# Optimization experiments

Measured on AMD Instinct MI355X. Metric: run time of the kernel, lower is better.

## Reference

```python
import jax, jax.numpy as jnp
import numpy as np

BN_EPS = 1e-5
# regular 3x3 kernel grid offsets: row0 = dy, row1 = dx, kernel positions in row-major order
REG = jnp.array([[-1, -1, -1, 0, 0, 0, 1, 1, 1],
                 [-1,  0,  1, -1, 0, 1, -1, 0, 1]], dtype=jnp.float32)


def conv3x3(x, w, b):
    y = jax.lax.conv_general_dilated(x, w, window_strides=(1, 1),
                                     padding=((1, 1), (1, 1)),
                                     dimension_numbers=('NCHW', 'OIHW', 'NCHW'))
    return y + b[None, :, None, None]


def deform_conv3x3(x, dy, dx, w):
    # x: [N,C,H,W]; dy,dx: [N,9,H,W] per-kernel-tap offsets; w: [O,C,3,3]
    N, C, H, W = x.shape
    K = 9
    ky = jnp.repeat(jnp.arange(3), 3)   # [0,0,0,1,1,1,2,2,2]
    kx = jnp.tile(jnp.arange(3), 3)     # [0,1,2,0,1,2,0,1,2]
    # sampling positions: p = p_out - pad + k*dilation + offset (stride=1, pad=dil=1)
    py = dy + (jnp.arange(H) - 1)[None, None, :, None] + ky[None, :, None, None].astype(x.dtype)
    px = dx + (jnp.arange(W) - 1)[None, None, None, :] + kx[None, :, None, None].astype(x.dtype)
    y0 = jnp.floor(py)
    x0 = jnp.floor(px)
    wy = py - y0  # bilinear weights
    wx = px - x0
    y0i = y0.astype(jnp.int32)
    x0i = x0.astype(jnp.int32)
    nidx = jnp.arange(N)[:, None, None, None]

    def gather(yi, xi):
        valid = ((yi >= 0) & (yi < H) & (xi >= 0) & (xi < W)).astype(x.dtype)
        v = x[nidx, :, jnp.clip(yi, 0, H - 1), jnp.clip(xi, 0, W - 1)]  # [N,K,H,W,C]
        return v * valid[..., None]

    sampled = (gather(y0i,     x0i)     * ((1 - wy) * (1 - wx))[..., None]
             + gather(y0i,     x0i + 1) * ((1 - wy) * wx)[..., None]
             + gather(y0i + 1, x0i)     * (wy * (1 - wx))[..., None]
             + gather(y0i + 1, x0i + 1) * (wy * wx)[..., None])  # [N,K,H,W,C]
    O = w.shape[0]
    return jnp.einsum('nkhwc,ock->nohw', sampled, w.reshape(O, C, K))


def setup_inputs() -> dict:
    key = jax.random.key(0)
    ks = jax.random.split(key, 12)
    N, C, H, W = 2, 256, 96, 96
    O = 256
    sc = 1.0 / np.sqrt(C * 9)
    return {
        'x': jax.random.normal(ks[0], (N, C, H, W), jnp.float32),
        'mask_attention': jax.random.normal(ks[1], (N, C, H, W), jnp.float32),
        'w_tm': jax.random.normal(ks[2], (4, C, 3, 3), jnp.float32) * sc,
        'b_tm': jax.random.normal(ks[3], (4,), jnp.float32) * 0.01,
        'w_tr': jax.random.normal(ks[4], (2, C, 3, 3), jnp.float32) * sc,
        'b_tr': jax.random.normal(ks[5], (2,), jnp.float32) * 0.01,
        'w_deform': jax.random.normal(ks[6], (O, C, 3, 3), jnp.float32) * sc,
        'bn_gamma': jnp.ones((O,), jnp.float32),
        'bn_beta': jnp.zeros((O,), jnp.float32),
        'bn_mean': jax.random.normal(ks[7], (O,), jnp.float32) * 0.01,
        'bn_var': jax.random.uniform(ks[8], (O,), jnp.float32, 0.5, 1.5),
    }


def reference(x, mask_attention, w_tm, b_tm, w_tr, b_tr, w_deform,
              bn_gamma, bn_beta, bn_mean, bn_var):
    # mask_attention is overwritten by x in the original forward; ignored.
    N, C, H, W = x.shape
    tm = conv3x3(x, w_tm, b_tm)                       # [N,4,H,W]
    T = tm.transpose(0, 2, 3, 1).reshape(N, H, W, 2, 2)
    off = jnp.einsum('nhwij,jk->nhwik', T, REG) - REG  # [N,H,W,2,9], (T-I)@REG
    tr = conv3x3(x, w_tr, b_tr)                        # [N,2,H,W]
    off = off + tr.transpose(0, 2, 3, 1)[..., None]    # broadcast translation to all 9 taps
    dy = off[..., 0, :].transpose(0, 3, 1, 2)          # [N,9,H,W]
    dx = off[..., 1, :].transpose(0, 3, 1, 2)
    out = deform_conv3x3(x, dy, dx, w_deform)          # [N,O,H,W]
    inv = jax.lax.rsqrt(bn_var + BN_EPS)
    out = (out - bn_mean[None, :, None, None]) * (inv * bn_gamma)[None, :, None, None] \
          + bn_beta[None, :, None, None]
    return jax.nn.relu(out + x)
```

## Files before the change

kernel.cpp:

```cpp
#include <hip/hip_runtime.h>
#include <stdint.h>

#define H_ 96
#define W_ 96
#define C_ 256
#define O_ 256
#define N_ 2
#define HW_ (H_*W_)
#define M_ (N_*HW_)
#define GK 2304

typedef _Float16 f16x8 __attribute__((ext_vector_type(8)));
typedef _Float16 f16x2 __attribute__((ext_vector_type(2)));
typedef float f32x4 __attribute__((ext_vector_type(4)));
typedef unsigned short us4 __attribute__((ext_vector_type(4)));
typedef unsigned short us8 __attribute__((ext_vector_type(8)));

__device__ __forceinline__ unsigned short f2h(float f) {
  union { _Float16 h; unsigned short u; } v;
  v.h = (_Float16)f;
  return v.u;
}
__device__ __forceinline__ f16x2 hpair(float f) {
  const _Float16 h = (_Float16)f;
  return (f16x2){h, h};
}

__global__ __launch_bounds__(256) void k_pre(const float* __restrict__ x,
                                             const float* __restrict__ w_df,
                                             const float* __restrict__ w_tm,
                                             const float* __restrict__ w_tr,
                                             unsigned short* __restrict__ xt,
                                             unsigned short* __restrict__ wfrag,
                                             unsigned short* __restrict__ w6p) {
  const int b = blockIdx.x;
  const int tid = threadIdx.x;
  if (b < 576) {
    __shared__ unsigned short tile[64][130];
    const int pt = b % 144;
    const int ch = (b / 144) & 1;
    const int n  = b / 288;
    const int p0 = pt * 64, c0 = ch * 128;
    const float* xp = x + (size_t)n * C_ * HW_;
    unsigned short* xtp = xt + (size_t)n * C_ * HW_;
    const int tx = tid & 15, ty = tid >> 4;
#pragma unroll
    for (int pass = 0; pass < 8; pass++) {
      const int c = pass * 16 + ty;
      const f32x4 v = *(const f32x4*)(xp + (size_t)(c0 + c) * HW_ + p0 + tx * 4);
#pragma unroll
      for (int i = 0; i < 4; i++) tile[tx * 4 + i][c] = f2h(v[i]);
    }
    __syncthreads();
    const int l32 = tid & 31, pr = tid >> 5;
#pragma unroll
    for (int pass = 0; pass < 8; pass++) {
      const int p = pass * 8 + pr;
      us4 v;
#pragma unroll
      for (int i = 0; i < 4; i++) v[i] = tile[p][l32 * 4 + i];
      *(us4*)(xtp + (size_t)(p0 + p) * C_ + c0 + l32 * 4) = v;
    }
  } else if (b < 864) {
    const int base = (b - 576) * 2048 + tid * 8;
    const int l  = (base >> 3) & 63;
    const int g  = (base >> 9) & 15;
    const int ks = (base >> 13) & 7;
    const int t  = base >> 16;
    const int o  = g * 16 + (l & 15);
    const int c  = ks * 32 + (l >> 4) * 8;
    us8 res;
#pragma unroll
    for (int j = 0; j < 8; j++) res[j] = f2h(w_df[(size_t)(o * 256 + c + j) * 9 + t]);
    *(us8*)(wfrag + base) = res;
  } else {
    int idx = (b - 864) * 256 + tid;
    int t = idx >> 12;
    int r = idx & 4095;
    int j = r >> 8;
    int c = r & 255;
    float v = 0.f;
    if (j < 4) v = w_tm[(size_t)(j * C_ + c) * 9 + t];
    else if (j < 6) v = w_tr[(size_t)((j - 4) * C_ + c) * 9 + t];
    w6p[idx] = f2h(v);
  }
}

__global__ __launch_bounds__(512, 2) void k_fused(const unsigned short* __restrict__ xt,
                                                  const unsigned short* __restrict__ Wfrag,
                                                  const unsigned short* __restrict__ w6p,
                                                  const float* __restrict__ b_tm,
                                                  const float* __restrict__ b_tr,
                                                  const float* __restrict__ xres,
                                                  const float* __restrict__ gamma,
                                                  const float* __restrict__ beta,
                                                  const float* __restrict__ mean,
                                                  const float* __restrict__ var,
                                                  float* __restrict__ out) {
  __shared__ unsigned short As[2][80 * 256] __attribute__((aligned(16)));
  __shared__ float sred5[5][8][16][8];
  __shared__ float coords_s[80][9][2];
  __shared__ int   nofs[80];
  const int tid = threadIdx.x;
  const int wave = tid >> 6, lane = tid & 63;
  const int row = lane & 15, quad = lane >> 4;
  const int pb = (blockIdx.x & 7) * 32 + (blockIdx.x >> 3);
  const bool fat = pb < 128;
  const int nt = fat ? 5 : 4;
  const int m0 = fat ? pb * 80 : 10240 + (pb - 128) * 64;
  const int sr = tid >> 4;
  const int cg = tid & 15;

#pragma unroll
  for (int t5 = 0; t5 < 5; ++t5) {
    if (t5 < nt) {
      const int ts = m0 + t5 * 16;
      const int nn = ts / HW_;
      const int hw = ts - nn * HW_;
      const int h = hw / W_, w0 = hw - h * W_;
      const unsigned short* xts = xt + (size_t)nn * C_ * HW_;
      const int cq = wave * 32;
      f32x4 oacc = {0.f, 0.f, 0.f, 0.f};
      const f16x8 zero8 = {};
#pragma unroll
      for (int t = 0; t < 9; t++) {
        const int ty = t / 3, tx = t % 3;
        const int y = h + ty - 1;
        if (y < 0 || y >= H_) continue;
        const int xx = w0 + row + tx - 1;
        const bool valid = (xx >= 0) && (xx < W_);
        const int xc = min(max(xx, 0), W_ - 1);
        f16x8 av = *(const f16x8*)(const void*)(xts + (size_t)(y * W_ + xc) * C_ + cq + quad * 8);
        if (!valid) av = zero8;
        const f16x8 bv = *(const f16x8*)(const void*)(w6p + (size_t)(t * 16 + row) * C_ + cq + quad * 8);
        oacc = __builtin_amdgcn_mfma_f32_16x16x32_f16(av, bv, oacc, 0, 0, 0);
      }
      if (row < 6) {
#pragma unroll
        for (int r = 0; r < 4; r++) sred5[t5][wave][quad * 4 + r][row] = oacc[r];
      }
    }
  }
  __syncthreads();
  if (tid < nt * 16) {
    const int rg = tid;
    const int gm = m0 + rg;
    const int nn = gm / HW_;
    const int hw = gm - nn * HW_;
    const int h = hw / W_, w = hw - h * W_;
    const int tt = rg >> 4, mm = rg & 15;
    float a[6];
#pragma unroll
    for (int j = 0; j < 6; j++) {
      float s = 0.f;
#pragma unroll
      for (int wv = 0; wv < 8; wv++) s += sred5[tt][wv][mm][j];
      a[j] = s;
    }
    const float tm0 = a[0] + b_tm[0];
    const float tm1 = a[1] + b_tm[1];
    const float tm2 = a[2] + b_tm[2];
    const float tm3 = a[3] + b_tm[3];
    const float tr0 = a[4] + b_tr[0];
    const float tr1 = a[5] + b_tr[1];
#pragma unroll
    for (int t = 0; t < 9; t++) {
      const float ry = (float)(t / 3) - 1.f;
      const float rx = (float)(t % 3) - 1.f;
      coords_s[rg][t][0] = (float)h + tr0 + tm0 * ry + tm1 * rx;
      coords_s[rg][t][1] = (float)w + tr1 + tm2 * ry + tm3 * rx;
    }
    nofs[rg] = nn * (C_ * HW_);
  }
  __syncthreads();

  f32x4 acc[5][2] = {};
  float cwA[4], cwB[4];
  us8 uA0[4], uA1[4], uB0[4], uB1[4];

#define ISSUE(S, R, TAP)                                                       \
  {                                                                            \
    const int r_ = (R);                                                        \
    const int nof = nofs[r_];                                                  \
    const float py = coords_s[r_][TAP][0];                                     \
    const float px = coords_s[r_][TAP][1];                                     \
    const float fy = floorf(py), fx = floorf(px);                              \
    const float wy = py - fy, wx = px - fx;                                    \
    const int y0 = (int)fy, x0 = (int)fx;                                      \
    const int y1 = y0 + 1, x1 = x0 + 1;                                        \
    const float vy0 = (y0 >= 0 && y0 < H_) ? 1.f : 0.f;                        \
    const float vy1 = (y1 >= 0 && y1 < H_) ? 1.f : 0.f;                        \
    const float vx0 = (x0 >= 0 && x0 < W_) ? 1.f : 0.f;                        \
    const float vx1 = (x1 >= 0 && x1 < W_) ? 1.f : 0.f;                        \
    cw##S[0] = (1.f - wy) * (1.f - wx) * vy0 * vx0;                            \
    cw##S[1] = (1.f - wy) * wx * vy0 * vx1;                                    \
    cw##S[2] = wy * (1.f - wx) * vy1 * vx0;                                    \
    cw##S[3] = wy * wx * vy1 * vx1;                                            \
    const int cy0 = min(max(y0, 0), H_ - 1), cy1 = min(max(y1, 0), H_ - 1);    \
    const int cx0 = min(max(x0, 0), W_ - 1), cx1 = min(max(x1, 0), W_ - 1);    \
    const int b0 = nof + (cy0 * W_ + cx0) * C_ + cg * 16;                      \
    const int b1 = nof + (cy0 * W_ + cx1) * C_ + cg * 16;                      \
    const int b2 = nof + (cy1 * W_ + cx0) * C_ + cg * 16;                      \
    const int b3 = nof + (cy1 * W_ + cx1) * C_ + cg * 16;                      \
    u##S##0[0] = *(const us8*)(xt + b0); u##S##1[0] = *(const us8*)(xt + b0 + 8); \
    u##S##0[1] = *(const us8*)(xt + b1); u##S##1[1] = *(const us8*)(xt + b1 + 8); \
    u##S##0[2] = *(const us8*)(xt + b2); u##S##1[2] = *(const us8*)(xt + b2 + 8); \
    u##S##0[3] = *(const us8*)(xt + b3); u##S##1[3] = *(const us8*)(xt + b3 + 8); \
  }

#define LERPW(S, R, ASB)                                                       \
  {                                                                            \
    const int r_ = (R);                                                        \
    const f16x2 c0 = hpair(cw##S[0]), c1 = hpair(cw##S[1]);                    \
    const f16x2 c2 = hpair(cw##S[2]), c3 = hpair(cw##S[3]);                    \
    us8 r0v, r1v;                                                              \
    {                                                                          \
      const f16x2* p0 = (const f16x2*)&u##S##0[0];                             \
      const f16x2* p1 = (const f16x2*)&u##S##0[1];                             \
      const f16x2* p2 = (const f16x2*)&u##S##0[2];                             \
      const f16x2* p3 = (const f16x2*)&u##S##0[3];                             \
      f16x2* d = (f16x2*)&r0v;                                                 \
      _Pragma("unroll")                                                        \
      for (int p = 0; p < 4; p++) {                                            \
        f16x2 r = p0[p] * c0; r = p1[p] * c1 + r;                              \
        r = p2[p] * c2 + r;   r = p3[p] * c3 + r;  d[p] = r;                   \
      }                                                                        \
    }                                                                          \
    {                                                                          \
      const f16x2* p0 = (const f16x2*)&u##S##1[0];                             \
      const f16x2* p1 = (const f16x2*)&u##S##1[1];                             \
      const f16x2* p2 = (const f16x2*)&u##S##1[2];                             \
      const f16x2* p3 = (const f16x2*)&u##S##1[3];                             \
      f16x2* d = (f16x2*)&r1v;                                                 \
      _Pragma("unroll")                                                        \
      for (int p = 0; p < 4; p++) {                                            \
        f16x2 r = p0[p] * c0; r = p1[p] * c1 + r;                              \
        r = p2[p] * c2 + r;   r = p3[p] * c3 + r;  d[p] = r;                   \
      }                                                                        \
    }                                                                          \
    const int q0i = cg * 2, q1i = cg * 2 + 1;                                  \
    const int s0 = (q0i & 24) | ((q0i ^ r_) & 7);                              \
    const int s1 = (q1i & 24) | ((q1i ^ r_) & 7);                              \
    *(us8*)(void*)&ASB[r_ * 256 + s0 * 8] = r0v;                               \
    *(us8*)(void*)&ASB[r_ * 256 + s1 * 8] = r1v;                               \
  }

  const bool third = fat && (sr < 16);

  ISSUE(A, sr, 0);
  __builtin_amdgcn_sched_barrier(0);

  for (int tap = 0; tap < 9; tap++) {
    unsigned short* __restrict__ asb = &As[tap & 1][0];

    ISSUE(B, sr + 32, tap);
    const unsigned short* wfTap =
        Wfrag + (size_t)tap * 65536 + wave * 1024 + lane * 8;
    f16x8 bv[2];
#pragma unroll
    for (int ot = 0; ot < 2; ot++) bv[ot] = *(const f16x8*)(const void*)(wfTap + ot * 512);
    __builtin_amdgcn_sched_barrier(0);

    LERPW(A, sr, asb);
    if (third) {
      ISSUE(A, sr + 64, tap);
      __builtin_amdgcn_sched_barrier(0);
    }
    LERPW(B, sr + 32, asb);
    if (third) LERPW(A, sr + 64, asb);

    __syncthreads();

    if (tap < 8) {
      ISSUE(A, sr, tap + 1);
      __builtin_amdgcn_sched_barrier(0);
    }

#pragma unroll
    for (int ks = 0; ks < 8; ks++) {
      const int q = ks * 4 + quad;
      const int slot = (q & 24) | ((q ^ row) & 7);
      f16x8 a0 = *(const f16x8*)(const void*)&asb[(0 * 16 + row) * 256 + slot * 8];
      f16x8 a1 = *(const f16x8*)(const void*)&asb[(1 * 16 + row) * 256 + slot * 8];
      f16x8 a2 = *(const f16x8*)(const void*)&asb[(2 * 16 + row) * 256 + slot * 8];
      f16x8 a3 = *(const f16x8*)(const void*)&asb[(3 * 16 + row) * 256 + slot * 8];
      f16x8 a4;
      if (fat) a4 = *(const f16x8*)(const void*)&asb[(4 * 16 + row) * 256 + slot * 8];
      f16x8 bn[2];
      if (ks < 7) {
        const unsigned short* wfn = wfTap + (size_t)(ks + 1) * 8192;
#pragma unroll
        for (int ot = 0; ot < 2; ot++) bn[ot] = *(const f16x8*)(const void*)(wfn + ot * 512);
      }
#pragma unroll
      for (int ot = 0; ot < 2; ot++) {
        acc[0][ot] = __builtin_amdgcn_mfma_f32_16x16x32_f16(a0, bv[ot], acc[0][ot], 0, 0, 0);
        acc[1][ot] = __builtin_amdgcn_mfma_f32_16x16x32_f16(a1, bv[ot], acc[1][ot], 0, 0, 0);
        acc[2][ot] = __builtin_amdgcn_mfma_f32_16x16x32_f16(a2, bv[ot], acc[2][ot], 0, 0, 0);
        acc[3][ot] = __builtin_amdgcn_mfma_f32_16x16x32_f16(a3, bv[ot], acc[3][ot], 0, 0, 0);
      }
      if (fat) {
#pragma unroll
        for (int ot = 0; ot < 2; ot++)
          acc[4][ot] = __builtin_amdgcn_mfma_f32_16x16x32_f16(a4, bv[ot], acc[4][ot], 0, 0, 0);
      }
      if (ks < 7) {
#pragma unroll
        for (int ot = 0; ot < 2; ot++) bv[ot] = bn[ot];
      }
    }
  }

#pragma unroll
  for (int ot = 0; ot < 2; ot++) {
    const int o = wave * 32 + ot * 16 + row;
    const float sc = rsqrtf(var[o] + 1e-5f) * gamma[o];
    const float bi = beta[o] - mean[o] * sc;
#pragma unroll
    for (int t5 = 0; t5 < 5; t5++) {
      if (t5 < nt) {
        const int ts = m0 + t5 * 16;
        const int nn = ts / HW_;
        const int hw0 = ts - nn * HW_ + quad * 4;
        const size_t ob = (size_t)(nn * O_ + o) * HW_ + hw0;
        const f32x4 rv = *(const f32x4*)(xres + ob);
        f32x4 ov;
#pragma unroll
        for (int r = 0; r < 4; r++) ov[r] = fmaxf(acc[t5][ot][r] * sc + bi + rv[r], 0.f);
        *(f32x4*)(out + ob) = ov;
      }
    }
  }
}

extern "C" void kernel_launch(void* const* d_in, const int* in_sizes, int n_in,
                              void* d_out, int out_size, void* d_ws, size_t ws_size,
                              hipStream_t stream) {
  const float* x     = (const float*)d_in[0];
  const float* w_tm  = (const float*)d_in[2];
  const float* b_tm  = (const float*)d_in[3];
  const float* w_tr  = (const float*)d_in[4];
  const float* b_tr  = (const float*)d_in[5];
  const float* w_df  = (const float*)d_in[6];
  const float* gamma = (const float*)d_in[7];
  const float* beta  = (const float*)d_in[8];
  const float* mean  = (const float*)d_in[9];
  const float* var   = (const float*)d_in[10];
  float* out = (float*)d_out;

  char* ws = (char*)d_ws;
  unsigned short* xt    = (unsigned short*)(ws);
  unsigned short* wfrag = (unsigned short*)(ws + 9437184);
  unsigned short* w6p   = (unsigned short*)(ws + 9437184 + 1179648);

  k_pre<<<1008, 256, 0, stream>>>(x, w_df, w_tm, w_tr, xt, wfrag, w6p);
  k_fused<<<256, 512, 0, stream>>>(xt, wfrag, w6p, b_tm, b_tr, x,
                                   gamma, beta, mean, var, out);
}
```

Baseline: 165.7 us.

## Double block to 1024 threads splitting M tiles across two wave halves

Launches the fused kernel with 1024 threads per block, giving 16 waves. Each half of the waves owns a subset of the 16-row M tiles (3+2 or 2+2) while keeping the same 8-way output-channel split. The bilinear gather and LDS staging are now spread over twice as many threads, so each thread fills one row (plus a third for fat blocks) instead of two or three, and per-thread accumulator and register state shrinks. The B-fragment prefetch becomes a two-deep ping-pong. The trade-off is that each weight fragment is now loaded twice per block, once per half, and the MFMA work per wave shrinks, which may reduce latency hiding per wave.

```diff
diff --git a/kernel.cpp b/kernel.cpp
--- a/kernel.cpp
+++ b/kernel.cpp
@@ -86,40 +86,43 @@
   }
 }
 
-__global__ __launch_bounds__(512, 2) void k_fused(const unsigned short* __restrict__ xt,
-                                                  const unsigned short* __restrict__ Wfrag,
-                                                  const unsigned short* __restrict__ w6p,
-                                                  const float* __restrict__ b_tm,
-                                                  const float* __restrict__ b_tr,
-                                                  const float* __restrict__ xres,
-                                                  const float* __restrict__ gamma,
-                                                  const float* __restrict__ beta,
-                                                  const float* __restrict__ mean,
-                                                  const float* __restrict__ var,
-                                                  float* __restrict__ out) {
+__global__ __launch_bounds__(1024) void k_fused(const unsigned short* __restrict__ xt,
+                                                const unsigned short* __restrict__ Wfrag,
+                                                const unsigned short* __restrict__ w6p,
+                                                const float* __restrict__ b_tm,
+                                                const float* __restrict__ b_tr,
+                                                const float* __restrict__ xres,
+                                                const float* __restrict__ gamma,
+                                                const float* __restrict__ beta,
+                                                const float* __restrict__ mean,
+                                                const float* __restrict__ var,
+                                                float* __restrict__ out) {
   __shared__ unsigned short As[2][80 * 256] __attribute__((aligned(16)));
   __shared__ float sred5[5][8][16][8];
   __shared__ float coords_s[80][9][2];
   __shared__ int   nofs[80];
   const int tid = threadIdx.x;
   const int wave = tid >> 6, lane = tid & 63;
+  const int w7 = wave & 7, half = wave >> 3;
   const int row = lane & 15, quad = lane >> 4;
   const int pb = (blockIdx.x & 7) * 32 + (blockIdx.x >> 3);
   const bool fat = pb < 128;
   const int nt = fat ? 5 : 4;
   const int m0 = fat ? pb * 80 : 10240 + (pb - 128) * 64;
+  const int tb  = half ? (fat ? 3 : 2) : 0;
+  const int ntw = half ? 2 : (fat ? 3 : 2);
   const int sr = tid >> 4;
   const int cg = tid & 15;
 
 #pragma unroll
   for (int t5 = 0; t5 < 5; ++t5) {
-    if (t5 < nt) {
+    if (t5 < nt && (t5 & 1) == half) {
       const int ts = m0 + t5 * 16;
       const int nn = ts / HW_;
       const int hw = ts - nn * HW_;
       const int h = hw / W_, w0 = hw - h * W_;
       const unsigned short* xts = xt + (size_t)nn * C_ * HW_;
-      const int cq = wave * 32;
+      const int cq = w7 * 32;
       f32x4 oacc = {0.f, 0.f, 0.f, 0.f};
       const f16x8 zero8 = {};
 #pragma unroll
@@ -137,7 +140,7 @@
       }
       if (row < 6) {
 #pragma unroll
-        for (int r = 0; r < 4; r++) sred5[t5][wave][quad * 4 + r][row] = oacc[r];
+        for (int r = 0; r < 4; r++) sred5[t5][w7][quad * 4 + r][row] = oacc[r];
       }
     }
   }
@@ -174,11 +177,11 @@
   }
   __syncthreads();
 
-  f32x4 acc[5][2] = {};
-  float cwA[4], cwB[4];
-  us8 uA0[4], uA1[4], uB0[4], uB1[4];
-
-#define ISSUE(S, R, TAP)                                                       \
+  f32x4 acc[3][2] = {};
+  float cwA[4];
+  us8 uA0[4], uA1[4];
+
+#define ISSUE(R, TAP)                                                          \
   {                                                                            \
     const int r_ = (R);                                                        \
     const int nof = nofs[r_];                                                  \
@@ -192,33 +195,33 @@
     const float vy1 = (y1 >= 0 && y1 < H_) ? 1.f : 0.f;                        \
     const float vx0 = (x0 >= 0 && x0 < W_) ? 1.f : 0.f;                        \
     const float vx1 = (x1 >= 0 && x1 < W_) ? 1.f : 0.f;                        \
-    cw##S[0] = (1.f - wy) * (1.f - wx) * vy0 * vx0;                            \
-    cw##S[1] = (1.f - wy) * wx * vy0 * vx1;                                    \
-    cw##S[2] = wy * (1.f - wx) * vy1 * vx0;                                    \
-    cw##S[3] = wy * wx * vy1 * vx1;                                            \
+    cwA[0] = (1.f - wy) * (1.f - wx) * vy0 * vx0;                              \
+    cwA[1] = (1.f - wy) * wx * vy0 * vx1;                                      \
+    cwA[2] = wy * (1.f - wx) * vy1 * vx0;                                      \
+    cwA[3] = wy * wx * vy1 * vx1;                                              \
     const int cy0 = min(max(y0, 0), H_ - 1), cy1 = min(max(y1, 0), H_ - 1);    \
     const int cx0 = min(max(x0, 0), W_ - 1), cx1 = min(max(x1, 0), W_ - 1);    \
     const int b0 = nof + (cy0 * W_ + cx0) * C_ + cg * 16;                      \
     const int b1 = nof + (cy0 * W_ + cx1) * C_ + cg * 16;                      \
     const int b2 = nof + (cy1 * W_ + cx0) * C_ + cg * 16;                      \
     const int b3 = nof + (cy1 * W_ + cx1) * C_ + cg * 16;                      \
-    u##S##0[0] = *(const us8*)(xt + b0); u##S##1[0] = *(const us8*)(xt + b0 + 8); \
-    u##S##0[1] = *(const us8*)(xt + b1); u##S##1[1] = *(const us8*)(xt + b1 + 8); \
-    u##S##0[2] = *(const us8*)(xt + b2); u##S##1[2] = *(const us8*)(xt + b2 + 8); \
-    u##S##0[3] = *(const us8*)(xt + b3); u##S##1[3] = *(const us8*)(xt + b3 + 8); \
-  }
-
-#define LERPW(S, R, ASB)                                                       \
+    uA0[0] = *(const us8*)(xt + b0); uA1[0] = *(const us8*)(xt + b0 + 8);      \
+    uA0[1] = *(const us8*)(xt + b1); uA1[1] = *(const us8*)(xt + b1 + 8);      \
+    uA0[2] = *(const us8*)(xt + b2); uA1[2] = *(const us8*)(xt + b2 + 8);      \
+    uA0[3] = *(const us8*)(xt + b3); uA1[3] = *(const us8*)(xt + b3 + 8);      \
+  }
+
+#define LERPW(R, ASB)                                                          \
   {                                                                            \
     const int r_ = (R);                                                        \
-    const f16x2 c0 = hpair(cw##S[0]), c1 = hpair(cw##S[1]);                    \
-    const f16x2 c2 = hpair(cw##S[2]), c3 = hpair(cw##S[3]);                    \
+    const f16x2 c0 = hpair(cwA[0]), c1 = hpair(cwA[1]);                        \
+    const f16x2 c2 = hpair(cwA[2]), c3 = hpair(cwA[3]);                        \
     us8 r0v, r1v;                                                              \
     {                                                                          \
-      const f16x2* p0 = (const f16x2*)&u##S##0[0];                             \
-      const f16x2* p1 = (const f16x2*)&u##S##0[1];                             \
-      const f16x2* p2 = (const f16x2*)&u##S##0[2];                             \
-      const f16x2* p3 = (const f16x2*)&u##S##0[3];                             \
+      const f16x2* p0 = (const f16x2*)&uA0[0];                                 \
+      const f16x2* p1 = (const f16x2*)&uA0[1];                                 \
+      const f16x2* p2 = (const f16x2*)&uA0[2];                                 \
+      const f16x2* p3 = (const f16x2*)&uA0[3];                                 \
       f16x2* d = (f16x2*)&r0v;                                                 \
       _Pragma("unroll")                                                        \
       for (int p = 0; p < 4; p++) {                                            \
@@ -227,10 +230,10 @@
       }                                                                        \
     }                                                                          \
     {                                                                          \
-      const f16x2* p0 = (const f16x2*)&u##S##1[0];                             \
-      const f16x2* p1 = (const f16x2*)&u##S##1[1];                             \
-      const f16x2* p2 = (const f16x2*)&u##S##1[2];                             \
-      const f16x2* p3 = (const f16x2*)&u##S##1[3];                             \
+      const f16x2* p0 = (const f16x2*)&uA1[0];                                 \
+      const f16x2* p1 = (const f16x2*)&uA1[1];                                 \
+      const f16x2* p2 = (const f16x2*)&uA1[2];                                 \
+      const f16x2* p3 = (const f16x2*)&uA1[3];                                 \
       f16x2* d = (f16x2*)&r1v;                                                 \
       _Pragma("unroll")                                                        \
       for (int p = 0; p < 4; p++) {                                            \
@@ -245,80 +248,80 @@
     *(us8*)(void*)&ASB[r_ * 256 + s1 * 8] = r1v;                               \
   }
 
+#define GS(KS, BX, BY)                                                         \
+  {                                                                            \
+    const int q = (KS) * 4 + quad;                                             \
+    const int slot = (q & 24) | ((q ^ row) & 7);                               \
+    f16x8 a0 = *(const f16x8*)(const void*)&asb[((tb + 0) * 16 + row) * 256 + slot * 8]; \
+    f16x8 a1 = *(const f16x8*)(const void*)&asb[((tb + 1) * 16 + row) * 256 + slot * 8]; \
+    f16x8 a2;                                                                  \
+    if (ntw > 2) a2 = *(const f16x8*)(const void*)&asb[((tb + 2) * 16 + row) * 256 + slot * 8]; \
+    f16x8 nx, ny;                                                              \
+    if ((KS) < 6) {                                                            \
+      const unsigned short* wfn = wfTap + (size_t)((KS) + 2) * 8192;           \
+      nx = *(const f16x8*)(const void*)(wfn);                                  \
+      ny = *(const f16x8*)(const void*)(wfn + 512);                            \
+    }                                                                          \
+    acc[0][0] = __builtin_amdgcn_mfma_f32_16x16x32_f16(a0, BX, acc[0][0], 0, 0, 0); \
+    acc[0][1] = __builtin_amdgcn_mfma_f32_16x16x32_f16(a0, BY, acc[0][1], 0, 0, 0); \
+    acc[1][0] = __builtin_amdgcn_mfma_f32_16x16x32_f16(a1, BX, acc[1][0], 0, 0, 0); \
+    acc[1][1] = __builtin_amdgcn_mfma_f32_16x16x32_f16(a1, BY, acc[1][1], 0, 0, 0); \
+    if (ntw > 2) {                                                             \
+      acc[2][0] = __builtin_amdgcn_mfma_f32_16x16x32_f16(a2, BX, acc[2][0], 0, 0, 0); \
+      acc[2][1] = __builtin_amdgcn_mfma_f32_16x16x32_f16(a2, BY, acc[2][1], 0, 0, 0); \
+    }                                                                          \
+    if ((KS) < 6) { BX = nx; BY = ny; }                                        \
+  }
+
   const bool third = fat && (sr < 16);
 
-  ISSUE(A, sr, 0);
+  ISSUE(sr, 0);
   __builtin_amdgcn_sched_barrier(0);
 
   for (int tap = 0; tap < 9; tap++) {
     unsigned short* __restrict__ asb = &As[tap & 1][0];
-
-    ISSUE(B, sr + 32, tap);
     const unsigned short* wfTap =
-        Wfrag + (size_t)tap * 65536 + wave * 1024 + lane * 8;
-    f16x8 bv[2];
-#pragma unroll
-    for (int ot = 0; ot < 2; ot++) bv[ot] = *(const f16x8*)(const void*)(wfTap + ot * 512);
+        Wfrag + (size_t)tap * 65536 + w7 * 1024 + lane * 8;
+
+    f16x8 B0 = *(const f16x8*)(const void*)(wfTap);
+    f16x8 B1 = *(const f16x8*)(const void*)(wfTap + 512);
+    f16x8 B2 = *(const f16x8*)(const void*)(wfTap + 8192);
+    f16x8 B3 = *(const f16x8*)(const void*)(wfTap + 8704);
     __builtin_amdgcn_sched_barrier(0);
 
-    LERPW(A, sr, asb);
+    LERPW(sr, asb);
     if (third) {
-      ISSUE(A, sr + 64, tap);
+      ISSUE(sr + 64, tap);
       __builtin_amdgcn_sched_barrier(0);
-    }
-    LERPW(B, sr + 32, asb);
-    if (third) LERPW(A, sr + 64, asb);
+      LERPW(sr + 64, asb);
+    }
 
     __syncthreads();
 
     if (tap < 8) {
-      ISSUE(A, sr, tap + 1);
+      ISSUE(sr, tap + 1);
       __builtin_amdgcn_sched_barrier(0);
     }
 
-#pragma unroll
-    for (int ks = 0; ks < 8; ks++) {
-      const int q = ks * 4 + quad;
-      const int slot = (q & 24) | ((q ^ row) & 7);
-      f16x8 a0 = *(const f16x8*)(const void*)&asb[(0 * 16 + row) * 256 + slot * 8];
-      f16x8 a1 = *(const f16x8*)(const void*)&asb[(1 * 16 + row) * 256 + slot * 8];
-      f16x8 a2 = *(const f16x8*)(const void*)&asb[(2 * 16 + row) * 256 + slot * 8];
-      f16x8 a3 = *(const f16x8*)(const void*)&asb[(3 * 16 + row) * 256 + slot * 8];
-      f16x8 a4;
-      if (fat) a4 = *(const f16x8*)(const void*)&asb[(4 * 16 + row) * 256 + slot * 8];
-      f16x8 bn[2];
-      if (ks < 7) {
-        const unsigned short* wfn = wfTap + (size_t)(ks + 1) * 8192;
-#pragma unroll
-        for (int ot = 0; ot < 2; ot++) bn[ot] = *(const f16x8*)(const void*)(wfn + ot * 512);
-      }
-#pragma unroll
-      for (int ot = 0; ot < 2; ot++) {
-        acc[0][ot] = __builtin_amdgcn_mfma_f32_16x16x32_f16(a0, bv[ot], acc[0][ot], 0, 0, 0);
-        acc[1][ot] = __builtin_amdgcn_mfma_f32_16x16x32_f16(a1, bv[ot], acc[1][ot], 0, 0, 0);
-        acc[2][ot] = __builtin_amdgcn_mfma_f32_16x16x32_f16(a2, bv[ot], acc[2][ot], 0, 0, 0);
-        acc[3][ot] = __builtin_amdgcn_mfma_f32_16x16x32_f16(a3, bv[ot], acc[3][ot], 0, 0, 0);
-      }
-      if (fat) {
-#pragma unroll
-        for (int ot = 0; ot < 2; ot++)
-          acc[4][ot] = __builtin_amdgcn_mfma_f32_16x16x32_f16(a4, bv[ot], acc[4][ot], 0, 0, 0);
-      }
-      if (ks < 7) {
-#pragma unroll
-        for (int ot = 0; ot < 2; ot++) bv[ot] = bn[ot];
-      }
-    }
+    GS(0, B0, B1)
+    GS(1, B2, B3)
+    GS(2, B0, B1)
+    GS(3, B2, B3)
+    GS(4, B0, B1)
+    GS(5, B2, B3)
+    GS(6, B0, B1)
+    GS(7, B2, B3)
   }
 
 #pragma unroll
   for (int ot = 0; ot < 2; ot++) {
-    const int o = wave * 32 + ot * 16 + row;
+    const int o = w7 * 32 + ot * 16 + row;
     const float sc = rsqrtf(var[o] + 1e-5f) * gamma[o];
     const float bi = beta[o] - mean[o] * sc;
 #pragma unroll
-    for (int t5 = 0; t5 < 5; t5++) {
-      if (t5 < nt) {
+    for (int i = 0; i < 3; i++) {
+      if (i < ntw) {
+        const int t5 = tb + i;
         const int ts = m0 + t5 * 16;
         const int nn = ts / HW_;
         const int hw0 = ts - nn * HW_ + quad * 4;
@@ -326,7 +329,7 @@
         const f32x4 rv = *(const f32x4*)(xres + ob);
         f32x4 ov;
 #pragma unroll
-        for (int r = 0; r < 4; r++) ov[r] = fmaxf(acc[t5][ot][r] * sc + bi + rv[r], 0.f);
+        for (int r = 0; r < 4; r++) ov[r] = fmaxf(acc[i][ot][r] * sc + bi + rv[r], 0.f);
         *(f32x4*)(out + ob) = ov;
       }
     }
@@ -354,6 +357,6 @@
   unsigned short* w6p   = (unsigned short*)(ws + 9437184 + 1179648);
 
   k_pre<<<1008, 256, 0, stream>>>(x, w_df, w_tm, w_tr, xt, wfrag, w6p);
-  k_fused<<<256, 512, 0, stream>>>(xt, wfrag, w6p, b_tm, b_tr, x,
-                                   gamma, beta, mean, var, out);
-}
+  k_fused<<<256, 1024, 0, stream>>>(xt, wfrag, w6p, b_tm, b_tr, x,
+                                    gamma, beta, mean, var, out);
+}
```

Measured after the change: 194.3 us. 1.17x slower.
